# Kernel tuning notes

Measured on AMD Instinct MI355X. Metric: run time of the kernel, lower is better.

Reference implementation:

```python
import jax, jax.numpy as jnp
import numpy as np

E, D_IN, D_OUT, N = 8, 1024, 1024, 8192

def setup_inputs() -> dict:
    key = jax.random.key(0)
    ks = jax.random.split(key, 5)
    s_in = 1.0 / np.sqrt(D_IN)
    x = jax.random.normal(ks[0], (N, D_IN), dtype=jnp.float32)
    We = jax.random.uniform(ks[1], (E, D_IN, D_OUT), dtype=jnp.float32, minval=-s_in, maxval=s_in)
    be = jax.random.uniform(ks[2], (E, D_OUT), dtype=jnp.float32, minval=-s_in, maxval=s_in)
    Wg = jax.random.uniform(ks[3], (D_IN, E), dtype=jnp.float32, minval=-s_in, maxval=s_in)
    bg = jax.random.uniform(ks[4], (E,), dtype=jnp.float32, minval=-s_in, maxval=s_in)
    return {"x": x, "We": We, "be": be, "Wg": Wg, "bg": bg}

def reference(x, We, be, Wg, bg):
    # experts_outputs: [N, E, D_OUT] (stacked per-expert Linear outputs)
    expert_out = jnp.einsum('ni,eio->neo', x, We) + be[None, :, :]
    # gate: softmax over experts, [N, E]
    gate = jax.nn.softmax(x @ Wg + bg, axis=1)
    # weighted combine (bmm of [N,1,E] x [N,E,D_OUT]) -> [N, D_OUT]
    return jnp.einsum('ne,neo->no', gate, expert_out)
```

## Files before the change

### kernel.cpp

```cpp
#include <hip/hip_runtime.h>
#include <hip/hip_bf16.h>
#include <cstdint>

#define NTOK 8192
#define DIN  1024
#define DOUT 1024
#define NEXP 8

typedef __attribute__((ext_vector_type(8)))  __bf16 bf16x8;
typedef __attribute__((ext_vector_type(4)))  float  f32x4;
typedef __attribute__((ext_vector_type(16))) float  f32x16;

__device__ __forceinline__ unsigned short f2bf(float f) {
    unsigned int u = __builtin_bit_cast(unsigned int, f);
    u += 0x7FFFu + ((u >> 16) & 1u);
    return (unsigned short)(u >> 16);
}

__device__ __forceinline__ void cp16(const void* gsrc, void* ldst) {
    __builtin_amdgcn_global_load_lds(
        (const __attribute__((address_space(1))) void*)gsrc,
        (__attribute__((address_space(3))) void*)ldst,
        16, 0, 0);
}

__global__ __launch_bounds__(256) void prep_kernel(
    const float* __restrict__ x, const float* __restrict__ We,
    const float* __restrict__ Wg, const float* __restrict__ bg,
    unsigned short* __restrict__ xb, unsigned short* __restrict__ wt,
    float* __restrict__ g)
{
    __shared__ float smem[12416];

    int t = threadIdx.x;

    if (blockIdx.x < 2048) {
        unsigned short* tile = (unsigned short*)smem;
        int b = blockIdx.x;
        int e  = b >> 8;
        int kt = (b >> 4) & 15;
        int ot = b & 15;

        const float* src = We + ((size_t)e << 20) + (size_t)(kt * 64) * DOUT + ot * 64;
        unsigned short* dst = wt + ((size_t)e << 20) + (size_t)(ot * 64) * DIN + kt * 64;

        int kl = t >> 2;
        int og = (t & 3) * 16;
#pragma unroll
        for (int c = 0; c < 4; ++c) {
            int o = og + c * 4;
            float4 v = *(const float4*)&src[(size_t)kl * DOUT + o];
            ushort4 u;
            u.x = f2bf(v.x); u.y = f2bf(v.y); u.z = f2bf(v.z); u.w = f2bf(v.w);
            *(ushort4*)&tile[kl * 72 + o] = u;
        }
        __syncthreads();
        int ol = t >> 2;
        int kg = (t & 3) * 16;
        unsigned short tmp[16];
#pragma unroll
        for (int i = 0; i < 16; ++i) tmp[i] = tile[(kg + i) * 72 + ol];
        *(uint4*)&dst[(size_t)ol * DIN + kg]     = *(uint4*)&tmp[0];
        *(uint4*)&dst[(size_t)ol * DIN + kg + 8] = *(uint4*)&tmp[8];
    } else {
        float* WgL = smem;
        float* xL  = smem + 8192;
        int n0 = (blockIdx.x - 2048) * 32;

#pragma unroll
        for (int q = 0; q < 8; ++q) {
            int fidx = q * 256 + t;
            int k  = fidx >> 1;
            int eh = (fidx & 1) * 4;
            float4 v = *(const float4*)&Wg[(size_t)k * 8 + eh];
            WgL[(eh + 0) * 1024 + k] = v.x;
            WgL[(eh + 1) * 1024 + k] = v.y;
            WgL[(eh + 2) * 1024 + k] = v.z;
            WgL[(eh + 3) * 1024 + k] = v.w;
        }

        int tt = t & 31;
        int e  = t >> 5;
        float acc = 0.f;

        for (int c = 0; c < 8; ++c) {
            int kb = c * 128;
#pragma unroll
            for (int q = 0; q < 4; ++q) {
                int fidx = q * 256 + t;
                int row = fidx >> 5;
                int kk  = (fidx & 31) * 4;
                float4 v = *(const float4*)&x[(size_t)(n0 + row) * DIN + kb + kk];
                ushort4 u;
                u.x = f2bf(v.x); u.y = f2bf(v.y); u.z = f2bf(v.z); u.w = f2bf(v.w);
                *(ushort4*)&xb[(size_t)(n0 + row) * DIN + kb + kk] = u;
                *(float4*)&xL[row * 132 + kk] = v;
            }
            __syncthreads();
#pragma unroll
            for (int kk = 0; kk < 128; kk += 4) {
                float4 xv = *(const float4*)&xL[tt * 132 + kk];
                float4 wv = *(const float4*)&WgL[e * 1024 + kb + kk];
                acc += xv.x * wv.x + xv.y * wv.y + xv.z * wv.z + xv.w * wv.w;
            }
            __syncthreads();
        }

        float* lg = xL;
        lg[tt * 8 + e] = acc + bg[e];
        __syncthreads();
        if (t < 32) {
            float l[8];
#pragma unroll
            for (int i = 0; i < 8; ++i) l[i] = lg[t * 8 + i];
            float m = l[0];
#pragma unroll
            for (int i = 1; i < 8; ++i) m = fmaxf(m, l[i]);
            float s = 0.f;
#pragma unroll
            for (int i = 0; i < 8; ++i) { l[i] = __expf(l[i] - m); s += l[i]; }
            float inv = 1.0f / s;
            float4 p0 = make_float4(l[0]*inv, l[1]*inv, l[2]*inv, l[3]*inv);
            float4 p1 = make_float4(l[4]*inv, l[5]*inv, l[6]*inv, l[7]*inv);
            *(float4*)&g[(size_t)(n0 + t) * 8]     = p0;
            *(float4*)&g[(size_t)(n0 + t) * 8 + 4] = p1;
        }
    }
}

__global__ __launch_bounds__(256, 2) void moe_gemm_kernel(
    const unsigned short* __restrict__ xb,
    const unsigned short* __restrict__ wt,
    const float* __restrict__ g,
    const float* __restrict__ be,
    float* __restrict__ out)
{
    __shared__ unsigned short lA[128 * 128];
    __shared__ unsigned short lB[128 * 128];

    int bid = blockIdx.x;
    int bm = (bid & 7) * 8 + ((bid >> 3) & 7);
    int bn = bid >> 6;
    int tid = threadIdx.x;
    int lane = tid & 63;
    int wave = tid >> 6;
    int wm = wave >> 1;
    int wn = wave & 1;

    const unsigned short* aBase = xb + (size_t)(bm * 128) * DIN;
    const unsigned short* bBase0 = wt + (size_t)(bn * 128) * DIN;

    int lrow  = lane >> 4;
    int cphys = lane & 15;
    int row7  = (((wave & 1) * 4) + lrow) & 7;
    int clog  = cphys ^ row7;

    int col  = lane & 31;
    int half = lane >> 5;

    f32x16 outAcc[2][2] = {};

#pragma unroll 1
    for (int e = 0; e < NEXP; ++e) {
        f32x16 acc[2][2] = {};
        const unsigned short* bBase = bBase0 + ((size_t)e << 20);

#pragma unroll 1
        for (int kt = 0; kt < 8; ++kt) {
            int kb = kt * 128;
            __syncthreads();
#pragma unroll
            for (int s = 0; s < 8; ++s) {
                int R0 = s * 16 + wave * 4;
                size_t srcOff = (size_t)(R0 + lrow) * DIN + kb + clog * 8;
                cp16(aBase + srcOff, &lA[R0 * 128]);
                cp16(bBase + srcOff, &lB[R0 * 128]);
            }
            __syncthreads();
#pragma unroll
            for (int ks = 0; ks < 8; ++ks) {
                int cl = ks * 2 + half;
                bf16x8 af[2], bfr[2];
#pragma unroll
                for (int i = 0; i < 2; ++i) {
                    int m = wm * 64 + i * 32 + col;
                    af[i] = *(const bf16x8*)&lA[m * 128 + (cl ^ (m & 7)) * 8];
                }
#pragma unroll
                for (int j = 0; j < 2; ++j) {
                    int o = wn * 64 + j * 32 + col;
                    bfr[j] = *(const bf16x8*)&lB[o * 128 + (cl ^ (o & 7)) * 8];
                }
#pragma unroll
                for (int i = 0; i < 2; ++i)
#pragma unroll
                    for (int j = 0; j < 2; ++j)
                        acc[i][j] = __builtin_amdgcn_mfma_f32_32x32x16_bf16(
                            af[i], bfr[j], acc[i][j], 0, 0, 0);
            }
        }

        float bv[2];
#pragma unroll
        for (int j = 0; j < 2; ++j)
            bv[j] = be[(size_t)e * DOUT + bn * 128 + wn * 64 + j * 32 + col];
#pragma unroll
        for (int i = 0; i < 2; ++i) {
#pragma unroll
            for (int q = 0; q < 4; ++q) {
                int rbase = bm * 128 + wm * 64 + i * 32 + q * 8 + half * 4;
                float g0 = g[(size_t)(rbase + 0) * 8 + e];
                float g1 = g[(size_t)(rbase + 1) * 8 + e];
                float g2 = g[(size_t)(rbase + 2) * 8 + e];
                float g3 = g[(size_t)(rbase + 3) * 8 + e];
#pragma unroll
                for (int j = 0; j < 2; ++j) {
                    outAcc[i][j][q * 4 + 0] += g0 * (acc[i][j][q * 4 + 0] + bv[j]);
                    outAcc[i][j][q * 4 + 1] += g1 * (acc[i][j][q * 4 + 1] + bv[j]);
                    outAcc[i][j][q * 4 + 2] += g2 * (acc[i][j][q * 4 + 2] + bv[j]);
                    outAcc[i][j][q * 4 + 3] += g3 * (acc[i][j][q * 4 + 3] + bv[j]);
                }
            }
        }
    }

#pragma unroll
    for (int i = 0; i < 2; ++i)
#pragma unroll
        for (int q = 0; q < 4; ++q) {
            int row = bm * 128 + wm * 64 + i * 32 + q * 8 + half * 4;
#pragma unroll
            for (int j = 0; j < 2; ++j) {
                int c = bn * 128 + wn * 64 + j * 32 + col;
#pragma unroll
                for (int r = 0; r < 4; ++r)
                    out[(size_t)(row + r) * DOUT + c] = outAcc[i][j][q * 4 + r];
            }
        }
}

extern "C" void kernel_launch(void* const* d_in, const int* in_sizes, int n_in,
                              void* d_out, int out_size, void* d_ws, size_t ws_size,
                              hipStream_t stream)
{
    const float* x  = (const float*)d_in[0];
    const float* We = (const float*)d_in[1];
    const float* be = (const float*)d_in[2];
    const float* Wg = (const float*)d_in[3];
    const float* bg = (const float*)d_in[4];
    float* out = (float*)d_out;

    unsigned short* xb = (unsigned short*)d_ws;
    unsigned short* wt = xb + (size_t)NTOK * DIN;
    float* g = (float*)(wt + (size_t)NEXP * DOUT * DIN);

    prep_kernel<<<2048 + 256, 256, 0, stream>>>(x, We, Wg, bg, xb, wt, g);
    moe_gemm_kernel<<<(NTOK / 128) * (DOUT / 128), 256, 0, stream>>>(xb, wt, g, be, out);
}
```

Measured before the change: 283.6 us.

## Process expert pairs per pass sharing A tile, use 16x16x32 MFMA

The GEMM now computes two experts at once, so each staged x tile in LDS feeds two weight tiles and A-tile global traffic and barriers per expert drop by half. K tiles shrink from 128 to 64 with a new XOR swizzle, and the MFMA changes from 32x32x16 to 16x16x32 with a 4x4 fragment layout per wave. Gate probabilities and biases are staged once in LDS instead of being read from global memory in each epilogue. The cost is doubled accumulator registers, which may hurt occupancy. The gate-row index in the prep kernel's softmax store also changes from t to tt, which may alter correctness.

```diff
diff --git a/kernel.cpp b/kernel.cpp
--- a/kernel.cpp
+++ b/kernel.cpp
@@ -9,7 +9,6 @@
 
 typedef __attribute__((ext_vector_type(8)))  __bf16 bf16x8;
 typedef __attribute__((ext_vector_type(4)))  float  f32x4;
-typedef __attribute__((ext_vector_type(16))) float  f32x16;
 
 __device__ __forceinline__ unsigned short f2bf(float f) {
     unsigned int u = __builtin_bit_cast(unsigned int, f);
@@ -122,8 +121,8 @@
             float inv = 1.0f / s;
             float4 p0 = make_float4(l[0]*inv, l[1]*inv, l[2]*inv, l[3]*inv);
             float4 p1 = make_float4(l[4]*inv, l[5]*inv, l[6]*inv, l[7]*inv);
-            *(float4*)&g[(size_t)(n0 + t) * 8]     = p0;
-            *(float4*)&g[(size_t)(n0 + t) * 8 + 4] = p1;
+            *(float4*)&g[(size_t)(n0 + tt) * 8]     = p0;
+            *(float4*)&g[(size_t)(n0 + tt) * 8 + 4] = p1;
         }
     }
 }
@@ -135,8 +134,11 @@
     const float* __restrict__ be,
     float* __restrict__ out)
 {
-    __shared__ unsigned short lA[128 * 128];
-    __shared__ unsigned short lB[128 * 128];
+    __shared__ unsigned short lA [128 * 64];
+    __shared__ unsigned short lB0[128 * 64];
+    __shared__ unsigned short lB1[128 * 64];
+    __shared__ float lG[128 * 8];
+    __shared__ float lBias[8 * 128];
 
     int bid = blockIdx.x;
     int bm = (bid & 7) * 8 + ((bid >> 3) & 7);
@@ -147,96 +149,106 @@
     int wm = wave >> 1;
     int wn = wave & 1;
 
+    {
+        *(float4*)&lG[tid * 4] = *(const float4*)&g[(size_t)(bm * 128) * 8 + tid * 4];
+#pragma unroll
+        for (int q = 0; q < 4; ++q) {
+            int idx = q * 256 + tid;
+            lBias[idx] = be[(size_t)(idx >> 7) * DOUT + bn * 128 + (idx & 127)];
+        }
+    }
+
+    f32x4 outAcc[4][4] = {};
+
     const unsigned short* aBase = xb + (size_t)(bm * 128) * DIN;
     const unsigned short* bBase0 = wt + (size_t)(bn * 128) * DIN;
 
-    int lrow  = lane >> 4;
-    int cphys = lane & 15;
-    int row7  = (((wave & 1) * 4) + lrow) & 7;
-    int clog  = cphys ^ row7;
-
-    int col  = lane & 31;
-    int half = lane >> 5;
-
-    f32x16 outAcc[2][2] = {};
-
-#pragma unroll 1
-    for (int e = 0; e < NEXP; ++e) {
-        f32x16 acc[2][2] = {};
-        const unsigned short* bBase = bBase0 + ((size_t)e << 20);
-
-#pragma unroll 1
-        for (int kt = 0; kt < 8; ++kt) {
-            int kb = kt * 128;
-            __syncthreads();
-#pragma unroll
-            for (int s = 0; s < 8; ++s) {
-                int R0 = s * 16 + wave * 4;
-                size_t srcOff = (size_t)(R0 + lrow) * DIN + kb + clog * 8;
-                cp16(aBase + srcOff, &lA[R0 * 128]);
-                cp16(bBase + srcOff, &lB[R0 * 128]);
-            }
-            __syncthreads();
-#pragma unroll
-            for (int ks = 0; ks < 8; ++ks) {
-                int cl = ks * 2 + half;
-                bf16x8 af[2], bfr[2];
-#pragma unroll
-                for (int i = 0; i < 2; ++i) {
-                    int m = wm * 64 + i * 32 + col;
-                    af[i] = *(const bf16x8*)&lA[m * 128 + (cl ^ (m & 7)) * 8];
+    int rowS = wave * 8 + (lane >> 3);
+    int k8   = (((lane & 7) ^ (lane >> 3)) * 8);
+    int rA   = lane & 15;
+    int swz  = rA & 7;
+
+    for (int ep = 0; ep < 4; ++ep) {
+        f32x4 acc0[4][4] = {};
+        f32x4 acc1[4][4] = {};
+        const unsigned short* b0Base = bBase0 + ((size_t)(2 * ep) << 20);
+        const unsigned short* b1Base = b0Base + (1u << 20);
+
+        for (int kt = 0; kt < 16; ++kt) {
+            int kb = kt * 64;
+            __syncthreads();
+#pragma unroll
+            for (int j = 0; j < 4; ++j) {
+                int row = j * 32 + rowS;
+                size_t so = (size_t)row * DIN + kb + k8;
+                cp16(aBase  + so, &lA [j * 2048 + wave * 512]);
+                cp16(b0Base + so, &lB0[j * 2048 + wave * 512]);
+                cp16(b1Base + so, &lB1[j * 2048 + wave * 512]);
+            }
+            __syncthreads();
+#pragma unroll
+            for (int ks = 0; ks < 2; ++ks) {
+                int kc = ks * 4 + (lane >> 4);
+                int kp = (kc ^ swz) * 8;
+                bf16x8 af[4], b0f[4], b1f[4];
+#pragma unroll
+                for (int i = 0; i < 4; ++i)
+                    af[i] = *(const bf16x8*)&lA[(wm * 64 + i * 16 + rA) * 64 + kp];
+#pragma unroll
+                for (int j = 0; j < 4; ++j) {
+                    b0f[j] = *(const bf16x8*)&lB0[(wn * 64 + j * 16 + rA) * 64 + kp];
+                    b1f[j] = *(const bf16x8*)&lB1[(wn * 64 + j * 16 + rA) * 64 + kp];
                 }
 #pragma unroll
-                for (int j = 0; j < 2; ++j) {
-                    int o = wn * 64 + j * 32 + col;
-                    bfr[j] = *(const bf16x8*)&lB[o * 128 + (cl ^ (o & 7)) * 8];
+                for (int i = 0; i < 4; ++i)
+#pragma unroll
+                    for (int j = 0; j < 4; ++j) {
+                        acc0[i][j] = __builtin_amdgcn_mfma_f32_16x16x32_bf16(
+                            af[i], b0f[j], acc0[i][j], 0, 0, 0);
+                        acc1[i][j] = __builtin_amdgcn_mfma_f32_16x16x32_bf16(
+                            af[i], b1f[j], acc1[i][j], 0, 0, 0);
+                    }
+            }
+        }
+
+#pragma unroll
+        for (int h = 0; h < 2; ++h) {
+            int e = 2 * ep + h;
+            f32x4 (*acc)[4] = h ? acc1 : acc0;
+            float bv[4];
+#pragma unroll
+            for (int j = 0; j < 4; ++j)
+                bv[j] = lBias[e * 128 + wn * 64 + j * 16 + rA];
+#pragma unroll
+            for (int i = 0; i < 4; ++i) {
+                int rb = wm * 64 + i * 16 + (lane >> 4) * 4;
+                float g0 = lG[(rb + 0) * 8 + e];
+                float g1 = lG[(rb + 1) * 8 + e];
+                float g2 = lG[(rb + 2) * 8 + e];
+                float g3 = lG[(rb + 3) * 8 + e];
+#pragma unroll
+                for (int j = 0; j < 4; ++j) {
+                    outAcc[i][j].x += g0 * (acc[i][j].x + bv[j]);
+                    outAcc[i][j].y += g1 * (acc[i][j].y + bv[j]);
+                    outAcc[i][j].z += g2 * (acc[i][j].z + bv[j]);
+                    outAcc[i][j].w += g3 * (acc[i][j].w + bv[j]);
                 }
-#pragma unroll
-                for (int i = 0; i < 2; ++i)
-#pragma unroll
-                    for (int j = 0; j < 2; ++j)
-                        acc[i][j] = __builtin_amdgcn_mfma_f32_32x32x16_bf16(
-                            af[i], bfr[j], acc[i][j], 0, 0, 0);
-            }
-        }
-
-        float bv[2];
-#pragma unroll
-        for (int j = 0; j < 2; ++j)
-            bv[j] = be[(size_t)e * DOUT + bn * 128 + wn * 64 + j * 32 + col];
-#pragma unroll
-        for (int i = 0; i < 2; ++i) {
-#pragma unroll
-            for (int q = 0; q < 4; ++q) {
-                int rbase = bm * 128 + wm * 64 + i * 32 + q * 8 + half * 4;
-                float g0 = g[(size_t)(rbase + 0) * 8 + e];
-                float g1 = g[(size_t)(rbase + 1) * 8 + e];
-                float g2 = g[(size_t)(rbase + 2) * 8 + e];
-                float g3 = g[(size_t)(rbase + 3) * 8 + e];
-#pragma unroll
-                for (int j = 0; j < 2; ++j) {
-                    outAcc[i][j][q * 4 + 0] += g0 * (acc[i][j][q * 4 + 0] + bv[j]);
-                    outAcc[i][j][q * 4 + 1] += g1 * (acc[i][j][q * 4 + 1] + bv[j]);
-                    outAcc[i][j][q * 4 + 2] += g2 * (acc[i][j][q * 4 + 2] + bv[j]);
-                    outAcc[i][j][q * 4 + 3] += g3 * (acc[i][j][q * 4 + 3] + bv[j]);
-                }
-            }
-        }
-    }
-
-#pragma unroll
-    for (int i = 0; i < 2; ++i)
-#pragma unroll
-        for (int q = 0; q < 4; ++q) {
-            int row = bm * 128 + wm * 64 + i * 32 + q * 8 + half * 4;
-#pragma unroll
-            for (int j = 0; j < 2; ++j) {
-                int c = bn * 128 + wn * 64 + j * 32 + col;
-#pragma unroll
-                for (int r = 0; r < 4; ++r)
-                    out[(size_t)(row + r) * DOUT + c] = outAcc[i][j][q * 4 + r];
-            }
-        }
+            }
+        }
+    }
+
+#pragma unroll
+    for (int i = 0; i < 4; ++i) {
+        int rowb = bm * 128 + wm * 64 + i * 16 + (lane >> 4) * 4;
+#pragma unroll
+        for (int j = 0; j < 4; ++j) {
+            int col = bn * 128 + wn * 64 + j * 16 + rA;
+            out[(size_t)(rowb + 0) * DOUT + col] = outAcc[i][j].x;
+            out[(size_t)(rowb + 1) * DOUT + col] = outAcc[i][j].y;
+            out[(size_t)(rowb + 2) * DOUT + col] = outAcc[i][j].z;
+            out[(size_t)(rowb + 3) * DOUT + col] = outAcc[i][j].w;
+        }
+    }
 }
 
 extern "C" void kernel_launch(void* const* d_in, const int* in_sizes, int n_in,
```

Result: slower. 383.6 us (+35.3%).
